# Optimization experiments

Hardware: AMD Instinct MI355X
Metric: run time of the kernel (lower is better)

The kernel has to match this reference:

```python
import math
import jax, jax.numpy as jnp
import numpy as np

B, T, E, H = 2, 2048, 1024, 16
HS = E // H  # head size = 64
NEG = jnp.float32(-1e10)


def setup_inputs() -> dict:
    key = jax.random.key(0)
    ks = jax.random.split(key, 7)
    return {
        "query": jax.random.normal(ks[0], (B, T, E), jnp.float32),
        "key": jax.random.normal(ks[1], (B, T, E), jnp.float32),
        "value": jax.random.normal(ks[2], (B, T, E), jnp.float32),
        "Wq": jax.random.normal(ks[3], (E, E), jnp.float32) * 0.02,
        "Wk": jax.random.normal(ks[4], (E, E), jnp.float32) * 0.02,
        "Wv": jax.random.normal(ks[5], (E, E), jnp.float32) * 0.02,
        "Wp": jax.random.normal(ks[6], (E, E), jnp.float32) * 0.02,
    }


def reference(query, key, value, Wq, Wk, Wv, Wp):
    # QKV projections (no bias), split into heads: [B, H, T, HS]
    q = (query @ Wq).reshape(B, T, H, HS).transpose(0, 2, 1, 3)
    k = (key @ Wk).reshape(B, T, H, HS).transpose(0, 2, 1, 3)
    v = (value @ Wv).reshape(B, T, H, HS).transpose(0, 2, 1, 3)
    # scaled dot-product scores [B, H, T, T]
    att = jnp.einsum("bhqd,bhkd->bhqk", q, k) / math.sqrt(HS)
    # additive causal mask (tril allowed)
    causal = jnp.tril(jnp.ones((T, T), dtype=att.dtype))
    att = att + jnp.where(causal == 0, NEG, jnp.float32(0.0))[None, None]
    att = jax.nn.softmax(att, axis=-1)
    # dropout rate 0 / deterministic -> identity
    y = jnp.einsum("bhqk,bhkd->bhqd", att, v)
    y = y.transpose(0, 2, 1, 3).reshape(B, T, E)
    y = y @ Wp
    return y
```

## Files before the change

kernel.cpp:

```cpp
#include <hip/hip_runtime.h>

#define TB 2
#define TT 2048
#define TE 1024
#define TH 16
#define THS 64
#define TM (TB * TT)

typedef __attribute__((ext_vector_type(8))) short short8;
typedef __attribute__((ext_vector_type(4))) float f32x4;
typedef __attribute__((ext_vector_type(16))) float f32x16;

__device__ __forceinline__ f32x4 mfma16(short8 a, short8 b, f32x4 c) {
    return __builtin_amdgcn_mfma_f32_16x16x32_bf16(a, b, c, 0, 0, 0);
}
__device__ __forceinline__ f32x16 mfma32(short8 a, short8 b, f32x16 c) {
    return __builtin_amdgcn_mfma_f32_32x32x16_bf16(a, b, c, 0, 0, 0);
}

__device__ __forceinline__ void gload_lds16(const void* g, void* l) {
    __builtin_amdgcn_global_load_lds(
        (const __attribute__((address_space(1))) void*)g,
        (__attribute__((address_space(3))) void*)l, 16, 0, 0);
}

__device__ __forceinline__ unsigned short f2bf(float f) {
    unsigned int u = __float_as_uint(f);
    u += 0x7fff + ((u >> 16) & 1);
    return (unsigned short)(u >> 16);
}

__device__ __forceinline__ unsigned cvtpk_bf16(float lo, float hi) {
    unsigned r;
    asm("v_cvt_pk_bf16_f32 %0, %1, %2" : "=v"(r) : "v"(lo), "v"(hi));
    return r;
}
__device__ __forceinline__ void plswap(unsigned& a, unsigned& b) {
    asm("v_permlane32_swap_b32 %0, %1" : "+v"(a), "+v"(b));
}

__global__ __launch_bounds__(256) void prep(
    const float* __restrict__ q, const float* __restrict__ k,
    const float* __restrict__ v, unsigned short* __restrict__ qc,
    unsigned short* __restrict__ kc, unsigned short* __restrict__ vc,
    const float* __restrict__ W0, const float* __restrict__ W1,
    const float* __restrict__ W2, const float* __restrict__ W3,
    unsigned short* __restrict__ T0, unsigned short* __restrict__ T1,
    unsigned short* __restrict__ T2, unsigned short* __restrict__ T3) {
    __shared__ float Ts[32][33];
    const int y = blockIdx.y;
    if (y < 3) {
        const float* src = (y == 0) ? q : (y == 1) ? k : v;
        unsigned short* dst = (y == 0) ? qc : (y == 1) ? kc : vc;
        const int i = blockIdx.x * 256 + threadIdx.x;
        float4 vv = ((const float4*)src)[i];
        ushort4 o;
        o.x = f2bf(vv.x); o.y = f2bf(vv.y); o.z = f2bf(vv.z); o.w = f2bf(vv.w);
        ((ushort4*)dst)[i] = o;
    } else {
        const int x = blockIdx.x;
        const int z = x >> 10, rem = x & 1023;
        const float* W = (z == 0) ? W0 : (z == 1) ? W1 : (z == 2) ? W2 : W3;
        unsigned short* Wt = (z == 0) ? T0 : (z == 1) ? T1 : (z == 2) ? T2 : T3;
        const int r0 = ((rem >> 5) & 31) * 32, c0 = (rem & 31) * 32;
        const int t = threadIdx.x;
        const int r = t >> 3, c = (t & 7) * 4;
        float4 vv = *(const float4*)&W[(size_t)(r0 + r) * TE + c0 + c];
        Ts[r][c] = vv.x; Ts[r][c + 1] = vv.y; Ts[r][c + 2] = vv.z; Ts[r][c + 3] = vv.w;
        __syncthreads();
        ushort4 o;
        o.x = f2bf(Ts[c + 0][r]); o.y = f2bf(Ts[c + 1][r]);
        o.z = f2bf(Ts[c + 2][r]); o.w = f2bf(Ts[c + 3][r]);
        *(ushort4*)&Wt[(size_t)(c0 + r) * TE + r0 + c] = o;
    }
}

__global__ __launch_bounds__(256, 2) void gemm_qkv(
    const unsigned short* __restrict__ qc, const unsigned short* __restrict__ kc,
    const unsigned short* __restrict__ vc, const unsigned short* __restrict__ Wqt,
    const unsigned short* __restrict__ Wkt, const unsigned short* __restrict__ Wvt,
    unsigned short* __restrict__ Qb, unsigned short* __restrict__ Kb,
    unsigned short* __restrict__ Vt) {
    __shared__ unsigned short LDS[32768];

    const int lin = blockIdx.x;
    const int swz = (lin & 7) * 96 + (lin >> 3);
    const int z = swz >> 8;
    const int rem = swz & 255;
    const int bm = (rem & 31) * 128, bn = (rem >> 5) * 128;

    const unsigned short* A  = (z == 0) ? qc : (z == 1) ? kc : vc;
    const unsigned short* Bt = (z == 0) ? Wqt : (z == 1) ? Wkt : Wvt;

    const int tid = threadIdx.x;
    const int w = tid >> 6, lane = tid & 63;
    const int quad = lane >> 4, l16 = lane & 15;
    const int wm = (w >> 1) * 64, wn = (w & 1) * 64;

    const int srow = lane >> 2;
    const int scol = (((lane & 3) ^ ((srow >> 1) & 3))) * 8;
    const int rchunk = (quad ^ ((l16 >> 1) & 3)) * 8;

    f32x4 acc[4][4];
    const f32x4 fz = {0.f, 0.f, 0.f, 0.f};
    #pragma unroll
    for (int i = 0; i < 4; ++i)
        #pragma unroll
        for (int j = 0; j < 4; ++j) acc[i][j] = fz;

    auto stageA = [&](int t, int half) {
        const int buf = t & 1, k0 = t * 64;
        #pragma unroll
        for (int j = 0; j < 2; ++j) {
            const int e = w * 2 + j;
            const int kk = e >> 2, i2 = e & 3;
            const int cr = half * 2 + (i2 & 1) + ((i2 >> 1) << 2);
            gload_lds16(A + (size_t)(bm + cr * 16 + srow) * TE + k0 + kk * 32 + scol,
                        &LDS[buf * 8192 + kk * 4096 + cr * 512 + lane * 8]);
        }
    };
    auto stageB = [&](int t, int half) {
        const int buf = t & 1, k0 = t * 64;
        #pragma unroll
        for (int j = 0; j < 2; ++j) {
            const int e = w * 2 + j;
            const int kk = e >> 2, i2 = e & 3;
            const int cc = half * 2 + (i2 & 1) + ((i2 >> 1) << 2);
            gload_lds16(Bt + (size_t)(bn + cc * 16 + srow) * TE + k0 + kk * 32 + scol,
                        &LDS[16384 + buf * 8192 + kk * 4096 + cc * 512 + lane * 8]);
        }
    };

    auto ktile = [&](int t, bool st, bool last) {
        const int buf = t & 1;
        const unsigned short* Al = &LDS[buf * 8192];
        const unsigned short* Bl = &LDS[16384 + buf * 8192];
        short8 af[2][2], blo[2][2], bhi[2][2];
        #pragma unroll
        for (int mi = 0; mi < 2; ++mi)
            #pragma unroll
            for (int kk = 0; kk < 2; ++kk)
                af[mi][kk] = *(const short8*)&Al[kk * 4096 + ((w >> 1) * 4 + mi) * 512 + l16 * 32 + rchunk];
        #pragma unroll
        for (int nj = 0; nj < 2; ++nj)
            #pragma unroll
            for (int kk = 0; kk < 2; ++kk)
                blo[nj][kk] = *(const short8*)&Bl[kk * 4096 + ((w & 1) * 4 + nj) * 512 + l16 * 32 + rchunk];
        asm volatile("s_waitcnt lgkmcnt(0)" ::: "memory");
        __builtin_amdgcn_sched_barrier(0);
        __builtin_amdgcn_s_setprio(1);
        #pragma unroll
        for (int mi = 0; mi < 2; ++mi)
            #pragma unroll
            for (int nj = 0; nj < 2; ++nj)
                #pragma unroll
                for (int kk = 0; kk < 2; ++kk)
                    acc[mi][nj] = mfma16(af[mi][kk], blo[nj][kk], acc[mi][nj]);
        __builtin_amdgcn_s_setprio(0);
        __builtin_amdgcn_sched_barrier(0);
        __builtin_amdgcn_s_barrier();
        #pragma unroll
        for (int nj = 0; nj < 2; ++nj)
            #pragma unroll
            for (int kk = 0; kk < 2; ++kk)
                bhi[nj][kk] = *(const short8*)&Bl[kk * 4096 + ((w & 1) * 4 + 2 + nj) * 512 + l16 * 32 + rchunk];
        if (st) { stageA(t + 2, 0); stageB(t + 2, 0); }
        asm volatile("s_waitcnt lgkmcnt(0)" ::: "memory");
        __builtin_amdgcn_sched_barrier(0);
        __builtin_amdgcn_s_setprio(1);
        #pragma unroll
        for (int mi = 0; mi < 2; ++mi)
            #pragma unroll
            for (int nj = 0; nj < 2; ++nj)
                #pragma unroll
                for (int kk = 0; kk < 2; ++kk)
                    acc[mi][2 + nj] = mfma16(af[mi][kk], bhi[nj][kk], acc[mi][2 + nj]);
        __builtin_amdgcn_s_setprio(0);
        __builtin_amdgcn_sched_barrier(0);
        __builtin_amdgcn_s_barrier();
        #pragma unroll
        for (int mi = 0; mi < 2; ++mi)
            #pragma unroll
            for (int kk = 0; kk < 2; ++kk)
                af[mi][kk] = *(const short8*)&Al[kk * 4096 + ((w >> 1) * 4 + 2 + mi) * 512 + l16 * 32 + rchunk];
        if (st) stageB(t + 2, 1);
        asm volatile("s_waitcnt lgkmcnt(0)" ::: "memory");
        __builtin_amdgcn_sched_barrier(0);
        __builtin_amdgcn_s_setprio(1);
        #pragma unroll
        for (int mi = 0; mi < 2; ++mi)
            #pragma unroll
            for (int nj = 0; nj < 2; ++nj)
                #pragma unroll
                for (int kk = 0; kk < 2; ++kk)
                    acc[2 + mi][nj] = mfma16(af[mi][kk], blo[nj][kk], acc[2 + mi][nj]);
        __builtin_amdgcn_s_setprio(0);
        __builtin_amdgcn_sched_barrier(0);
        __builtin_amdgcn_s_barrier();
        if (st) stageA(t + 2, 1);
        __builtin_amdgcn_s_setprio(1);
        #pragma unroll
        for (int mi = 0; mi < 2; ++mi)
            #pragma unroll
            for (int nj = 0; nj < 2; ++nj)
                #pragma unroll
                for (int kk = 0; kk < 2; ++kk)
                    acc[2 + mi][2 + nj] = mfma16(af[mi][kk], bhi[nj][kk], acc[2 + mi][2 + nj]);
        __builtin_amdgcn_s_setprio(0);
        __builtin_amdgcn_sched_barrier(0);
        if (st) {
            asm volatile("s_waitcnt vmcnt(8)" ::: "memory");
        } else if (last) {
            asm volatile("s_waitcnt vmcnt(0)" ::: "memory");
        }
        __builtin_amdgcn_s_barrier();
    };

    stageA(0, 0); stageB(0, 0); stageB(0, 1); stageA(0, 1);
    stageA(1, 0); stageB(1, 0); stageB(1, 1); stageA(1, 1);
    asm volatile("s_waitcnt vmcnt(8)" ::: "memory");
    __builtin_amdgcn_s_barrier();

    #pragma unroll 1
    for (int t = 0; t < 14; ++t) ktile(t, true, false);
    ktile(14, false, true);
    ktile(15, false, false);

    if (z < 2) {
        unsigned short* Cb = (z == 0) ? Qb : Kb;
        const float sc = (z == 0) ? 0.18033688011112042f : 1.0f;
        #pragma unroll
        for (int mi = 0; mi < 4; ++mi)
            #pragma unroll
            for (int nj = 0; nj < 4; ++nj) {
                const int m0 = bm + wm + mi * 16 + quad * 4;
                const int n = bn + wn + nj * 16 + l16;
                #pragma unroll
                for (int r = 0; r < 4; ++r)
                    Cb[(size_t)(m0 + r) * TE + n] = f2bf(acc[mi][nj][r] * sc);
            }
    } else {
        #pragma unroll
        for (int mi = 0; mi < 4; ++mi)
            #pragma unroll
            for (int nj = 0; nj < 4; ++nj) {
                const int m0 = bm + wm + mi * 16 + quad * 4;
                const int n = bn + wn + nj * 16 + l16;
                ushort4 o;
                o.x = f2bf(acc[mi][nj][0]); o.y = f2bf(acc[mi][nj][1]);
                o.z = f2bf(acc[mi][nj][2]); o.w = f2bf(acc[mi][nj][3]);
                size_t idx = ((size_t)((m0 >> 11) * TH + (n >> 6)) * THS + (n & 63)) * TT + (m0 & (TT - 1));
                *(ushort4*)&Vt[idx] = o;
            }
    }
}

__global__ __launch_bounds__(256, 2) void gemm_out(
    const unsigned short* __restrict__ A, const unsigned short* __restrict__ Bt,
    float* __restrict__ C) {
    __shared__ unsigned short As[2][128 * 32];
    __shared__ unsigned short Bs[2][64 * 32];

    const int tid = threadIdx.x;
    const int w = tid >> 6, lane = tid & 63;
    const int quad = lane >> 4, l16 = lane & 15;
    const int bm = blockIdx.x * 128, bn = blockIdx.y * 64;
    const int wm = (w >> 1) * 64, wn = (w & 1) * 32;

    f32x4 acc[4][2];
    const f32x4 fz = {0.f, 0.f, 0.f, 0.f};
    #pragma unroll
    for (int i = 0; i < 4; ++i)
        #pragma unroll
        for (int j = 0; j < 2; ++j) acc[i][j] = fz;

    const int srow = lane >> 2;
    const int scol = (((lane & 3) ^ ((srow >> 1) & 3))) * 8;
    const int rchunk = (quad ^ ((l16 >> 1) & 3)) * 8;

    auto stage = [&](int k0, int buf) {
        #pragma unroll
        for (int i = 0; i < 3; ++i) {
            const int ch = w * 3 + i;
            if (ch < 8)
                gload_lds16(A + (size_t)(bm + ch * 16 + srow) * TE + k0 + scol,
                            &As[buf][ch * 512 + lane * 8]);
            else
                gload_lds16(Bt + (size_t)(bn + (ch - 8) * 16 + srow) * TE + k0 + scol,
                            &Bs[buf][(ch - 8) * 512 + lane * 8]);
        }
    };

    stage(0, 0);
    int cur = 0;
    for (int k0 = 0; k0 < TE; k0 += 32) {
        __syncthreads();
        if (k0 + 32 < TE) stage(k0 + 32, cur ^ 1);

        short8 af[4], bf[2];
        #pragma unroll
        for (int i = 0; i < 4; ++i)
            af[i] = *(const short8*)&As[cur][(wm + i * 16 + l16) * 32 + rchunk];
        #pragma unroll
        for (int j = 0; j < 2; ++j)
            bf[j] = *(const short8*)&Bs[cur][(wn + j * 16 + l16) * 32 + rchunk];
        #pragma unroll
        for (int i = 0; i < 4; ++i)
            #pragma unroll
            for (int j = 0; j < 2; ++j)
                acc[i][j] = mfma16(af[i], bf[j], acc[i][j]);
        cur ^= 1;
    }

    #pragma unroll
    for (int i = 0; i < 4; ++i)
        #pragma unroll
        for (int j = 0; j < 2; ++j) {
            const int m0 = bm + wm + i * 16 + quad * 4;
            const int n = bn + wn + j * 16 + l16;
            #pragma unroll
            for (int r = 0; r < 4; ++r)
                C[(size_t)(m0 + r) * TE + n] = acc[i][j][r];
        }
}

__global__ __launch_bounds__(512, 4) void attn_mfma(
    const unsigned short* __restrict__ Q, const unsigned short* __restrict__ K,
    const unsigned short* __restrict__ Vt, unsigned short* __restrict__ O) {
    __shared__ unsigned short S[32768];
    __shared__ float L0[128];

    const int tid = threadIdx.x;
    const int lane = tid & 63;
    const int wv = tid >> 6;
    const int wk = wv >> 2;
    const int wl = wv & 3;
    const int rl = lane & 31, x = lane >> 5;

    const int lin = blockIdx.x;
    const int bh = lin & 31;
    const int it = 15 - (lin >> 5);
    const int b = bh >> 4, h = bh & 15;
    const int h0 = it + 1;
    const int base = wk ? h0 : 0;

    const unsigned short* Kg = K + (size_t)b * TT * TE + h * THS;
    const unsigned short* Vg = Vt + (size_t)bh * THS * TT;

    short8 aq[4];
    {
        const size_t rQ = (size_t)(b * TT + it * 128 + wl * 32 + rl) * TE + h * THS + x * 8;
        #pragma unroll
        for (int c = 0; c < 4; ++c) aq[c] = *(const short8*)&Q[rQ + c * 16];
    }

    const int srow = lane >> 2;
    const int scol = (((lane & 3) ^ ((srow >> 1) & 3))) * 8;
    unsigned short* Sg = S + wk * 16384;

    auto stage = [&](int jt, int buf) {
        const int k0 = jt * 64;
        if (wl < 2) {
            #pragma unroll
            for (int j = 0; j < 4; ++j) {
                const int ee = wl * 4 + j;
                const int kk = ee >> 2, r16 = (ee & 3) * 16;
                gload_lds16(Kg + (size_t)(k0 + r16 + srow) * TE + kk * 32 + scol,
                            &Sg[buf * 4096 + ee * 512 + lane * 8]);
            }
        } else {
            #pragma unroll
            for (int j = 0; j < 4; ++j) {
                const int ee = (wl - 2) * 4 + j;
                const int kk = ee >> 2, r16 = (ee & 3) * 16;
                gload_lds16(Vg + (size_t)(r16 + srow) * TT + k0 + kk * 32 + scol,
                            &Sg[8192 + buf * 4096 + ee * 512 + lane * 8]);
            }
        }
    };

    stage(base, 0);

    const int xr = (rl >> 1) & 3;
    const int q0 = it * 128;
    const int qv = q0 + wl * 32 + rl;
    const int qwMin = q0 + wl * 32;

    f32x16 accO0, accO1;
    #pragma unroll
    for (int i = 0; i < 16; ++i) { accO0[i] = 0.f; accO1[i] = 0.f; }
    float lacc = 0.f;

    #pragma unroll 1
    for (int i = 0; i < h0; ++i) {
        const int buf = i & 1;
        asm volatile("s_waitcnt vmcnt(0)" ::: "memory");
        __builtin_amdgcn_s_barrier();
        __builtin_amdgcn_sched_barrier(0);
        if (i + 1 < h0) stage(base + i + 1, buf ^ 1);

        const int jt = base + i;
        const int k0 = jt * 64;
        const unsigned short* Kb = &Sg[buf * 4096];
        const unsigned short* Vb = &Sg[8192 + buf * 4096];

        f32x16 sa0, sa1;
        #pragma unroll
        for (int i2 = 0; i2 < 16; ++i2) { sa0[i2] = 0.f; sa1[i2] = 0.f; }
        #pragma unroll
        for (int c = 0; c < 4; ++c) {
            const int off = (c >> 1) * 2048 + ((((c & 1) * 2 + x) ^ xr)) * 8;
            short8 kf0 = *(const short8*)&Kb[off + rl * 32];
            short8 kf1 = *(const short8*)&Kb[off + (32 + rl) * 32];
            sa0 = mfma32(kf0, aq[c], sa0);
            sa1 = mfma32(kf1, aq[c], sa1);
        }

        const bool open = (k0 + 63 <= qwMin);
        short8 pb[4];
        float lp0 = 0.f, lp1 = 0.f, lp2 = 0.f, lp3 = 0.f;
        #pragma unroll
        for (int mt = 0; mt < 2; ++mt) {
            float pv[16];
            #pragma unroll
            for (int r = 0; r < 16; ++r) {
                const float sv = (mt == 0) ? sa0[r] : sa1[r];
                float e = __builtin_amdgcn_exp2f(sv);
                if (!open) {
                    const int kg = k0 + mt * 32 + (r & 3) + 8 * (r >> 2) + 4 * x;
                    e = (kg > qv) ? 0.f : e;
                }
                pv[r] = e;
                if ((r & 3) == 0) lp0 += e;
                else if ((r & 3) == 1) lp1 += e;
                else if ((r & 3) == 2) lp2 += e;
                else lp3 += e;
            }
            unsigned w0 = cvtpk_bf16(pv[0], pv[1]),   w1 = cvtpk_bf16(pv[2], pv[3]);
            unsigned w2 = cvtpk_bf16(pv[4], pv[5]),   w3 = cvtpk_bf16(pv[6], pv[7]);
            unsigned w4 = cvtpk_bf16(pv[8], pv[9]),   w5 = cvtpk_bf16(pv[10], pv[11]);
            unsigned w6 = cvtpk_bf16(pv[12], pv[13]), w7 = cvtpk_bf16(pv[14], pv[15]);
            plswap(w0, w2); plswap(w1, w3);
            plswap(w4, w6); plswap(w5, w7);
            union { unsigned u[4]; short8 s8; } f0, f1;
            f0.u[0] = w0; f0.u[1] = w1; f0.u[2] = w2; f0.u[3] = w3;
            f1.u[0] = w4; f1.u[1] = w5; f1.u[2] = w6; f1.u[3] = w7;
            pb[mt * 2] = f0.s8; pb[mt * 2 + 1] = f1.s8;
        }
        lacc += (lp0 + lp1) + (lp2 + lp3);

        __builtin_amdgcn_s_setprio(1);
        #pragma unroll
        for (int c = 0; c < 4; ++c) {
            const int off = (c >> 1) * 2048 + ((((c & 1) * 2 + x) ^ xr)) * 8;
            short8 vf0 = *(const short8*)&Vb[off + rl * 32];
            short8 vf1 = *(const short8*)&Vb[off + (32 + rl) * 32];
            accO0 = mfma32(vf0, pb[c], accO0);
            accO1 = mfma32(vf1, pb[c], accO1);
        }
        __builtin_amdgcn_s_setprio(0);
    }

    lacc += __shfl_xor(lacc, 32);

    __syncthreads();
    float* Sf = (float*)S;
    if (wk == 0) {
        #pragma unroll
        for (int dt = 0; dt < 2; ++dt)
            #pragma unroll
            for (int q4 = 0; q4 < 4; ++q4) {
                const int i16 = ((dt ^ ((lane >> 2) & 1)) << 4) + ((q4 ^ (lane & 3)) << 2);
                const int flat = (wl * 64 + lane) * 32 + i16;
                float4 vstv;
                if (dt == 0) { vstv.x = accO0[q4*4+0]; vstv.y = accO0[q4*4+1]; vstv.z = accO0[q4*4+2]; vstv.w = accO0[q4*4+3]; }
                else         { vstv.x = accO1[q4*4+0]; vstv.y = accO1[q4*4+1]; vstv.z = accO1[q4*4+2]; vstv.w = accO1[q4*4+3]; }
                *(float4*)&Sf[flat] = vstv;
            }
        if (lane < 32) L0[wl * 32 + rl] = lacc;
    }
    __syncthreads();
    if (wk == 1) {
        const float lf = lacc + L0[wl * 32 + rl];
        const float linv = 1.0f / lf;
        unsigned short* Og = O + (size_t)(b * TT + q0 + wl * 32 + rl) * TE + h * THS;
        #pragma unroll
        for (int dt = 0; dt < 2; ++dt)
            #pragma unroll
            for (int q4 = 0; q4 < 4; ++q4) {
                const int i16 = ((dt ^ ((lane >> 2) & 1)) << 4) + ((q4 ^ (lane & 3)) << 2);
                const int flat = (wl * 64 + lane) * 32 + i16;
                const float4 vld = *(const float4*)&Sf[flat];
                float o0, o1, o2, o3;
                if (dt == 0) { o0 = accO0[q4*4+0] + vld.x; o1 = accO0[q4*4+1] + vld.y; o2 = accO0[q4*4+2] + vld.z; o3 = accO0[q4*4+3] + vld.w; }
                else         { o0 = accO1[q4*4+0] + vld.x; o1 = accO1[q4*4+1] + vld.y; o2 = accO1[q4*4+2] + vld.z; o3 = accO1[q4*4+3] + vld.w; }
                const int dbase = 8 * q4 + 4 * x + 32 * dt;
                ushort4 o;
                o.x = f2bf(o0 * linv); o.y = f2bf(o1 * linv);
                o.z = f2bf(o2 * linv); o.w = f2bf(o3 * linv);
                *(ushort4*)&Og[dbase] = o;
            }
    }
}

extern "C" void kernel_launch(void* const* d_in, const int* in_sizes, int n_in,
                              void* d_out, int out_size, void* d_ws, size_t ws_size,
                              hipStream_t stream) {
    const float* q  = (const float*)d_in[0];
    const float* k  = (const float*)d_in[1];
    const float* v  = (const float*)d_in[2];
    const float* Wq = (const float*)d_in[3];
    const float* Wk = (const float*)d_in[4];
    const float* Wv = (const float*)d_in[5];
    const float* Wp = (const float*)d_in[6];
    float* out = (float*)d_out;

    const size_t se = (size_t)TM * TE;
    unsigned short* qc  = (unsigned short*)d_ws;
    unsigned short* kc  = qc + se;
    unsigned short* vc  = kc + se;
    unsigned short* Qb  = vc + se;
    unsigned short* Kb  = Qb + se;
    unsigned short* Vt  = Kb + se;
    unsigned short* Ob  = Vt + se;
    unsigned short* Wqt = Ob + se;
    unsigned short* Wkt = Wqt + (size_t)TE * TE;
    unsigned short* Wvt = Wkt + (size_t)TE * TE;
    unsigned short* Wpt = Wvt + (size_t)TE * TE;

    prep<<<dim3(4096, 4), 256, 0, stream>>>(q, k, v, qc, kc, vc,
                                            Wq, Wk, Wv, Wp, Wqt, Wkt, Wvt, Wpt);

    gemm_qkv<<<768, 256, 0, stream>>>(qc, kc, vc, Wqt, Wkt, Wvt, Qb, Kb, Vt);

    attn_mfma<<<512, 512, 0, stream>>>(Qb, Kb, Vt, Ob);

    gemm_out<<<dim3(TM / 128, TE / 64), 256, 0, stream>>>(Ob, Wpt, out);
}
```

Before: 208.0 us.

## Replace split-KV two-group attention blocks with single 4-wave blocks processing paired KV tiles

The attention kernel drops the split of each query tile's KV range across two 4-wave groups, which needed a shared-memory reduction of partial outputs and row sums at the end. Each block now has 4 waves that stage two 64-key tiles per iteration into a double buffer and walk the whole causal range themselves, skipping sub-tiles that lie entirely above the diagonal. This removes the cross-group reduction and its barriers. In exchange each block runs a serial loop that is up to twice as long, with half as many waves per block, which may reduce latency hiding and parallelism across the grid.

```diff
diff --git a/kernel.cpp b/kernel.cpp
--- a/kernel.cpp
+++ b/kernel.cpp
@@ -324,25 +324,21 @@
         }
 }
 
-__global__ __launch_bounds__(512, 4) void attn_mfma(
+__global__ __launch_bounds__(256, 2) void attn_mfma(
     const unsigned short* __restrict__ Q, const unsigned short* __restrict__ K,
     const unsigned short* __restrict__ Vt, unsigned short* __restrict__ O) {
     __shared__ unsigned short S[32768];
-    __shared__ float L0[128];
 
     const int tid = threadIdx.x;
     const int lane = tid & 63;
-    const int wv = tid >> 6;
-    const int wk = wv >> 2;
-    const int wl = wv & 3;
+    const int wl = tid >> 6;
     const int rl = lane & 31, x = lane >> 5;
 
     const int lin = blockIdx.x;
     const int bh = lin & 31;
     const int it = 15 - (lin >> 5);
     const int b = bh >> 4, h = bh & 15;
-    const int h0 = it + 1;
-    const int base = wk ? h0 : 0;
+    const int nt = it + 1;
 
     const unsigned short* Kg = K + (size_t)b * TT * TE + h * THS;
     const unsigned short* Vg = Vt + (size_t)bh * THS * TT;
@@ -356,151 +352,129 @@
 
     const int srow = lane >> 2;
     const int scol = (((lane & 3) ^ ((srow >> 1) & 3))) * 8;
-    unsigned short* Sg = S + wk * 16384;
-
-    auto stage = [&](int jt, int buf) {
-        const int k0 = jt * 64;
-        if (wl < 2) {
-            #pragma unroll
-            for (int j = 0; j < 4; ++j) {
-                const int ee = wl * 4 + j;
+
+    auto stage = [&](int p, int buf) {
+        const int sub = wl >> 1;
+        const int k0 = (2 * p + sub) * 64;
+        if ((wl & 1) == 0) {
+            #pragma unroll
+            for (int ee = 0; ee < 8; ++ee) {
                 const int kk = ee >> 2, r16 = (ee & 3) * 16;
                 gload_lds16(Kg + (size_t)(k0 + r16 + srow) * TE + kk * 32 + scol,
-                            &Sg[buf * 4096 + ee * 512 + lane * 8]);
+                            &S[buf * 16384 + sub * 4096 + ee * 512 + lane * 8]);
             }
         } else {
             #pragma unroll
-            for (int j = 0; j < 4; ++j) {
-                const int ee = (wl - 2) * 4 + j;
+            for (int ee = 0; ee < 8; ++ee) {
                 const int kk = ee >> 2, r16 = (ee & 3) * 16;
                 gload_lds16(Vg + (size_t)(r16 + srow) * TT + k0 + kk * 32 + scol,
-                            &Sg[8192 + buf * 4096 + ee * 512 + lane * 8]);
+                            &S[buf * 16384 + 8192 + sub * 4096 + ee * 512 + lane * 8]);
             }
         }
     };
 
-    stage(base, 0);
+    stage(0, 0);
 
     const int xr = (rl >> 1) & 3;
     const int q0 = it * 128;
     const int qv = q0 + wl * 32 + rl;
     const int qwMin = q0 + wl * 32;
-
-    f32x16 accO0, accO1;
+    const int qwMax = qwMin + 31;
+
+    f32x16 accO0, accO1, fz16;
     #pragma unroll
-    for (int i = 0; i < 16; ++i) { accO0[i] = 0.f; accO1[i] = 0.f; }
+    for (int i = 0; i < 16; ++i) { accO0[i] = 0.f; accO1[i] = 0.f; fz16[i] = 0.f; }
     float lacc = 0.f;
 
     #pragma unroll 1
-    for (int i = 0; i < h0; ++i) {
+    for (int i = 0; i < nt; ++i) {
         const int buf = i & 1;
         asm volatile("s_waitcnt vmcnt(0)" ::: "memory");
         __builtin_amdgcn_s_barrier();
         __builtin_amdgcn_sched_barrier(0);
-        if (i + 1 < h0) stage(base + i + 1, buf ^ 1);
-
-        const int jt = base + i;
-        const int k0 = jt * 64;
-        const unsigned short* Kb = &Sg[buf * 4096];
-        const unsigned short* Vb = &Sg[8192 + buf * 4096];
-
-        f32x16 sa0, sa1;
-        #pragma unroll
-        for (int i2 = 0; i2 < 16; ++i2) { sa0[i2] = 0.f; sa1[i2] = 0.f; }
-        #pragma unroll
-        for (int c = 0; c < 4; ++c) {
-            const int off = (c >> 1) * 2048 + ((((c & 1) * 2 + x) ^ xr)) * 8;
-            short8 kf0 = *(const short8*)&Kb[off + rl * 32];
-            short8 kf1 = *(const short8*)&Kb[off + (32 + rl) * 32];
-            sa0 = mfma32(kf0, aq[c], sa0);
-            sa1 = mfma32(kf1, aq[c], sa1);
-        }
-
-        const bool open = (k0 + 63 <= qwMin);
-        short8 pb[4];
-        float lp0 = 0.f, lp1 = 0.f, lp2 = 0.f, lp3 = 0.f;
-        #pragma unroll
-        for (int mt = 0; mt < 2; ++mt) {
-            float pv[16];
-            #pragma unroll
-            for (int r = 0; r < 16; ++r) {
-                const float sv = (mt == 0) ? sa0[r] : sa1[r];
-                float e = __builtin_amdgcn_exp2f(sv);
-                if (!open) {
-                    const int kg = k0 + mt * 32 + (r & 3) + 8 * (r >> 2) + 4 * x;
-                    e = (kg > qv) ? 0.f : e;
+        if (i + 1 < nt) stage(i + 1, buf ^ 1);
+
+        #pragma unroll
+        for (int sub = 0; sub < 2; ++sub) {
+            const int k0 = (2 * i + sub) * 64;
+            if (k0 > qwMax) continue;
+
+            const unsigned short* Kb = &S[buf * 16384 + sub * 4096];
+            const unsigned short* Vb = &S[buf * 16384 + 8192 + sub * 4096];
+
+            f32x16 sa0 = fz16, sa1 = fz16;
+            #pragma unroll
+            for (int c = 0; c < 4; ++c) {
+                const int off = (c >> 1) * 2048 + ((((c & 1) * 2 + x) ^ xr)) * 8;
+                short8 kf0 = *(const short8*)&Kb[off + rl * 32];
+                short8 kf1 = *(const short8*)&Kb[off + (32 + rl) * 32];
+                sa0 = mfma32(kf0, aq[c], sa0);
+                sa1 = mfma32(kf1, aq[c], sa1);
+            }
+
+            const bool open = (k0 + 63 <= qwMin);
+            short8 pb[4];
+            float lp0 = 0.f, lp1 = 0.f, lp2 = 0.f, lp3 = 0.f;
+            #pragma unroll
+            for (int mt = 0; mt < 2; ++mt) {
+                float pv[16];
+                #pragma unroll
+                for (int r = 0; r < 16; ++r) {
+                    const float sv = (mt == 0) ? sa0[r] : sa1[r];
+                    float e = __builtin_amdgcn_exp2f(sv);
+                    if (!open) {
+                        const int kg = k0 + mt * 32 + (r & 3) + 8 * (r >> 2) + 4 * x;
+                        e = (kg > qv) ? 0.f : e;
+                    }
+                    pv[r] = e;
+                    if ((r & 3) == 0) lp0 += e;
+                    else if ((r & 3) == 1) lp1 += e;
+                    else if ((r & 3) == 2) lp2 += e;
+                    else lp3 += e;
                 }
-                pv[r] = e;
-                if ((r & 3) == 0) lp0 += e;
-                else if ((r & 3) == 1) lp1 += e;
-                else if ((r & 3) == 2) lp2 += e;
-                else lp3 += e;
-            }
-            unsigned w0 = cvtpk_bf16(pv[0], pv[1]),   w1 = cvtpk_bf16(pv[2], pv[3]);
-            unsigned w2 = cvtpk_bf16(pv[4], pv[5]),   w3 = cvtpk_bf16(pv[6], pv[7]);
-            unsigned w4 = cvtpk_bf16(pv[8], pv[9]),   w5 = cvtpk_bf16(pv[10], pv[11]);
-            unsigned w6 = cvtpk_bf16(pv[12], pv[13]), w7 = cvtpk_bf16(pv[14], pv[15]);
-            plswap(w0, w2); plswap(w1, w3);
-            plswap(w4, w6); plswap(w5, w7);
-            union { unsigned u[4]; short8 s8; } f0, f1;
-            f0.u[0] = w0; f0.u[1] = w1; f0.u[2] = w2; f0.u[3] = w3;
-            f1.u[0] = w4; f1.u[1] = w5; f1.u[2] = w6; f1.u[3] = w7;
-            pb[mt * 2] = f0.s8; pb[mt * 2 + 1] = f1.s8;
-        }
-        lacc += (lp0 + lp1) + (lp2 + lp3);
-
-        __builtin_amdgcn_s_setprio(1);
-        #pragma unroll
-        for (int c = 0; c < 4; ++c) {
-            const int off = (c >> 1) * 2048 + ((((c & 1) * 2 + x) ^ xr)) * 8;
-            short8 vf0 = *(const short8*)&Vb[off + rl * 32];
-            short8 vf1 = *(const short8*)&Vb[off + (32 + rl) * 32];
-            accO0 = mfma32(vf0, pb[c], accO0);
-            accO1 = mfma32(vf1, pb[c], accO1);
-        }
-        __builtin_amdgcn_s_setprio(0);
+                unsigned w0 = cvtpk_bf16(pv[0], pv[1]),   w1 = cvtpk_bf16(pv[2], pv[3]);
+                unsigned w2 = cvtpk_bf16(pv[4], pv[5]),   w3 = cvtpk_bf16(pv[6], pv[7]);
+                unsigned w4 = cvtpk_bf16(pv[8], pv[9]),   w5 = cvtpk_bf16(pv[10], pv[11]);
+                unsigned w6 = cvtpk_bf16(pv[12], pv[13]), w7 = cvtpk_bf16(pv[14], pv[15]);
+                plswap(w0, w2); plswap(w1, w3);
+                plswap(w4, w6); plswap(w5, w7);
+                union { unsigned u[4]; short8 s8; } f0, f1;
+                f0.u[0] = w0; f0.u[1] = w1; f0.u[2] = w2; f0.u[3] = w3;
+                f1.u[0] = w4; f1.u[1] = w5; f1.u[2] = w6; f1.u[3] = w7;
+                pb[mt * 2] = f0.s8; pb[mt * 2 + 1] = f1.s8;
+            }
+            lacc += (lp0 + lp1) + (lp2 + lp3);
+
+            __builtin_amdgcn_s_setprio(1);
+            #pragma unroll
+            for (int c = 0; c < 4; ++c) {
+                const int off = (c >> 1) * 2048 + ((((c & 1) * 2 + x) ^ xr)) * 8;
+                short8 vf0 = *(const short8*)&Vb[off + rl * 32];
+                short8 vf1 = *(const short8*)&Vb[off + (32 + rl) * 32];
+                accO0 = mfma32(vf0, pb[c], accO0);
+                accO1 = mfma32(vf1, pb[c], accO1);
+            }
+            __builtin_amdgcn_s_setprio(0);
+        }
     }
 
     lacc += __shfl_xor(lacc, 32);
-
-    __syncthreads();
-    float* Sf = (float*)S;
-    if (wk == 0) {
-        #pragma unroll
-        for (int dt = 0; dt < 2; ++dt)
-            #pragma unroll
-            for (int q4 = 0; q4 < 4; ++q4) {
-                const int i16 = ((dt ^ ((lane >> 2) & 1)) << 4) + ((q4 ^ (lane & 3)) << 2);
-                const int flat = (wl * 64 + lane) * 32 + i16;
-                float4 vstv;
-                if (dt == 0) { vstv.x = accO0[q4*4+0]; vstv.y = accO0[q4*4+1]; vstv.z = accO0[q4*4+2]; vstv.w = accO0[q4*4+3]; }
-                else         { vstv.x = accO1[q4*4+0]; vstv.y = accO1[q4*4+1]; vstv.z = accO1[q4*4+2]; vstv.w = accO1[q4*4+3]; }
-                *(float4*)&Sf[flat] = vstv;
-            }
-        if (lane < 32) L0[wl * 32 + rl] = lacc;
-    }
-    __syncthreads();
-    if (wk == 1) {
-        const float lf = lacc + L0[wl * 32 + rl];
-        const float linv = 1.0f / lf;
-        unsigned short* Og = O + (size_t)(b * TT + q0 + wl * 32 + rl) * TE + h * THS;
-        #pragma unroll
-        for (int dt = 0; dt < 2; ++dt)
-            #pragma unroll
-            for (int q4 = 0; q4 < 4; ++q4) {
-                const int i16 = ((dt ^ ((lane >> 2) & 1)) << 4) + ((q4 ^ (lane & 3)) << 2);
-                const int flat = (wl * 64 + lane) * 32 + i16;
-                const float4 vld = *(const float4*)&Sf[flat];
-                float o0, o1, o2, o3;
-                if (dt == 0) { o0 = accO0[q4*4+0] + vld.x; o1 = accO0[q4*4+1] + vld.y; o2 = accO0[q4*4+2] + vld.z; o3 = accO0[q4*4+3] + vld.w; }
-                else         { o0 = accO1[q4*4+0] + vld.x; o1 = accO1[q4*4+1] + vld.y; o2 = accO1[q4*4+2] + vld.z; o3 = accO1[q4*4+3] + vld.w; }
-                const int dbase = 8 * q4 + 4 * x + 32 * dt;
-                ushort4 o;
-                o.x = f2bf(o0 * linv); o.y = f2bf(o1 * linv);
-                o.z = f2bf(o2 * linv); o.w = f2bf(o3 * linv);
-                *(ushort4*)&Og[dbase] = o;
-            }
-    }
+    const float linv = 1.0f / lacc;
+
+    unsigned short* Og = O + (size_t)(b * TT + q0 + wl * 32 + rl) * TE + h * THS;
+    #pragma unroll
+    for (int dt = 0; dt < 2; ++dt)
+        #pragma unroll
+        for (int q4 = 0; q4 < 4; ++q4) {
+            float o0, o1, o2, o3;
+            if (dt == 0) { o0 = accO0[q4*4+0]; o1 = accO0[q4*4+1]; o2 = accO0[q4*4+2]; o3 = accO0[q4*4+3]; }
+            else         { o0 = accO1[q4*4+0]; o1 = accO1[q4*4+1]; o2 = accO1[q4*4+2]; o3 = accO1[q4*4+3]; }
+            const int dbase = 8 * q4 + 4 * x + 32 * dt;
+            ushort4 o;
+            o.x = f2bf(o0 * linv); o.y = f2bf(o1 * linv);
+            o.z = f2bf(o2 * linv); o.w = f2bf(o3 * linv);
+            *(ushort4*)&Og[dbase] = o;
+        }
 }
 
 extern "C" void kernel_launch(void* const* d_in, const int* in_sizes, int n_in,
@@ -533,7 +507,7 @@
 
     gemm_qkv<<<768, 256, 0, stream>>>(qc, kc, vc, Wqt, Wkt, Wvt, Qb, Kb, Vt);
 
-    attn_mfma<<<512, 512, 0, stream>>>(Qb, Kb, Vt, Ob);
+    attn_mfma<<<512, 256, 0, stream>>>(Qb, Kb, Vt, Ob);
 
     gemm_out<<<dim3(TM / 128, TE / 64), 256, 0, stream>>>(Ob, Wpt, out);
 }
```

Result: no change. 207.8 us (-0.1%).
